# Kernel tuning notes

Measured on AMD Instinct MI355X. Metric: run time of the kernel, lower is better.

Reference implementation:

```python
import jax, jax.numpy as jnp
import numpy as np

GAMMA = 2.0
EPS = 1e-06
LAMBDA_DISTANCE = 1.0
LAMBDA_NORMAL = 0.01
LAMBDA_LAPLACIAN = 0.1
CLS = 1


def vertex_normals(v, f, eps=EPS):
    # v: [N,3], f: [F,3] int. Scatter face normals to vertices, then normalize.
    fv = v[f]  # [F,3,3]
    fn = jnp.cross(fv[:, 1] - fv[:, 0], fv[:, 2] - fv[:, 0])  # [F,3]
    vn = jnp.zeros_like(v)
    vn = vn.at[f[:, 0]].add(fn).at[f[:, 1]].add(fn).at[f[:, 2]].add(fn)
    norm = jnp.maximum(jnp.linalg.norm(vn, axis=-1, keepdims=True), eps)
    return vn / norm


def squared_cdist(a, b):
    # [Na,3] x [Nb,3] -> squared euclidean distances [Na,Nb] (clamped >= 0)
    a2 = jnp.sum(a * a, axis=1)[:, None]
    b2 = jnp.sum(b * b, axis=1)[None, :]
    d2 = a2 + b2 - 2.0 * (a @ b.T)
    return jnp.maximum(d2, 0.0)


def sample_binary_targets(label, v, cls=CLS):
    # Nearest-neighbor grid_sample, align_corners=True, padding zeros.
    # grid = 2*v - 1 -> voxel index = round(v * (size-1)); v[:,0]->W, v[:,1]->H, v[:,2]->D.
    D, H, W = label.shape[2], label.shape[3], label.shape[4]
    ix = jnp.round(v[:, 0] * (W - 1)).astype(jnp.int32)
    iy = jnp.round(v[:, 1] * (H - 1)).astype(jnp.int32)
    iz = jnp.round(v[:, 2] * (D - 1)).astype(jnp.int32)
    inb = (ix >= 0) & (ix < W) & (iy >= 0) & (iy < H) & (iz >= 0) & (iz < D)
    ixc = jnp.clip(ix, 0, W - 1)
    iyc = jnp.clip(iy, 0, H - 1)
    izc = jnp.clip(iz, 0, D - 1)
    vals = (label[0, 0, izc, iyc, ixc] == cls).astype(jnp.float32)
    return jnp.where(inb, vals, 0.0)


def spatial_consistency_loss(rel_pos, targets, gamma=GAMMA, eps=EPS):
    p = jnp.clip(rel_pos, eps, 1.0 - eps)
    pos = targets > 0.5
    pc = jnp.sum(pos).astype(p.dtype)
    tot = jnp.asarray(p.shape[0], p.dtype)
    nc = tot - pc
    alpha = nc / (tot + eps)
    lpos = -alpha * jnp.power(1.0 - p, gamma) * jnp.log(p)
    lneg = -(1.0 - alpha) * jnp.power(p, gamma) * jnp.log(1.0 - p)
    return jnp.sum(jnp.where(pos, lpos, lneg)) / (tot + eps)


def laplacian_uniform(v, f):
    # Uniform mesh Laplacian smoothing: || mean(neighbors) - v ||, averaged.
    i = jnp.concatenate([f[:, 0], f[:, 1], f[:, 2], f[:, 1], f[:, 2], f[:, 0]])
    j = jnp.concatenate([f[:, 1], f[:, 2], f[:, 0], f[:, 0], f[:, 1], f[:, 2]])
    nsum = jnp.zeros_like(v).at[i].add(v[j])
    deg = jnp.zeros((v.shape[0],), v.dtype).at[i].add(1.0)
    lap = nsum / jnp.maximum(deg, 1.0)[:, None] - v
    return jnp.mean(jnp.linalg.norm(lap, axis=1))


def loss_forward(pred_vertices, relative_positions, gt_vertices, pred_faces, gt_faces, label):
    gt_v = jax.lax.stop_gradient(gt_vertices)  # gt comes from label volume; detached in original
    gt_normals = vertex_normals(gt_v, gt_faces)
    # spatial (focal-style) loss
    targets = sample_binary_targets(label, pred_vertices)
    spatial = spatial_consistency_loss(relative_positions, targets)
    # chamfer-style squared surface distance
    d2 = squared_cdist(pred_vertices, gt_v)  # [Np,Ng]
    distance = jnp.mean(jnp.min(d2, axis=1)) + jnp.mean(jnp.min(d2, axis=0))
    # normal consistency vs nearest gt vertex
    pred_normals = vertex_normals(pred_vertices, pred_faces)
    nearest = jnp.argmin(d2, axis=1)
    normal = jnp.mean((pred_normals - gt_normals[nearest]) ** 2)
    # uniform laplacian smoothing
    laplacian = laplacian_uniform(pred_vertices, pred_faces)
    total = spatial + LAMBDA_DISTANCE * distance + LAMBDA_NORMAL * normal + LAMBDA_LAPLACIAN * laplacian
    return total


def setup_inputs() -> dict:
    key = jax.random.key(0)
    k1, k2, k3, k4, k5, k6 = jax.random.split(key, 6)
    Np, Ng = 8192, 12000
    pred_vertices = jax.random.uniform(k1, (Np, 3), dtype=jnp.float32)
    relative_positions = jax.random.uniform(k2, (Np,), dtype=jnp.float32)
    gt_vertices = jax.random.uniform(k3, (Ng, 3), dtype=jnp.float32)
    pred_faces = jax.random.randint(k4, (2 * Np, 3), 0, Np, dtype=jnp.int32)
    gt_faces = jax.random.randint(k5, (2 * Ng, 3), 0, Ng, dtype=jnp.int32)
    label = jax.random.randint(k6, (1, 1, 96, 96, 96), 0, 2, dtype=jnp.int32)
    return {"pred_vertices": pred_vertices, "relative_positions": relative_positions,
            "gt_vertices": gt_vertices, "pred_faces": pred_faces,
            "gt_faces": gt_faces, "label": label}


def reference(pred_vertices, relative_positions, gt_vertices, pred_faces, gt_faces, label):
    return loss_forward(pred_vertices, relative_positions, gt_vertices, pred_faces, gt_faces, label)
```

## Files before the change

### kernel.cpp

```cpp
#include <hip/hip_runtime.h>
#include <math.h>

#define NP 8192
#define NG 12000
#define NFP 16384
#define NFG 24000
#define EPSF 1e-6f

#define GR 16
#define NC (GR*GR*GR)
#define HCELL 0.0625f
#define QL 16
#define QPB (256 / QL)
#define PRED_QBLOCKS (NP / QPB)
#define GT_QBLOCKS (NG / QPB)
#define FACE_BLOCKS ((NFG + NFP + 255) / 256)
#define QF_BLOCKS (PRED_QBLOCKS + GT_QBLOCKS + FACE_BLOCKS)
#define FIN_BLOCKS (NP / 256)

static constexpr size_t OFF_STARTP = 0;
static constexpr size_t OFF_STARTG = 16640;
static constexpr size_t OFF_SORTP  = 33280;
static constexpr size_t OFF_SORTG  = 164352;
static constexpr size_t OFF_GTN    = 356352;
static constexpr size_t OFF_PNN    = 500352;
static constexpr size_t OFF_NSUM   = 598656;
static constexpr size_t OFF_DEG    = 696960;
static constexpr size_t OFF_NEAR   = 729728;
static constexpr size_t OFF_ACCUM  = 762496;
static constexpr size_t OFF_DONE   = 762528;
#define N_ZERO 101545

__device__ __forceinline__ int cell_of(float x) {
    int c = (int)(x * (float)GR);
    return min(max(c, 0), GR - 1);
}

__device__ __forceinline__ void build_cells(const float* __restrict__ pts, int n,
                                            unsigned* __restrict__ start,
                                            float4* __restrict__ sorted,
                                            unsigned* h, unsigned* wsum) {
    int t = threadIdx.x;
    int lane = t & 63, wid = t >> 6;
    for (int i = t; i < NC; i += 1024) h[i] = 0u;
    __syncthreads();
    for (int i = t; i < n; i += 1024) {
        int c = (cell_of(pts[3*i+2]) * GR + cell_of(pts[3*i+1])) * GR + cell_of(pts[3*i]);
        atomicAdd(&h[c], 1u);
    }
    __syncthreads();
    unsigned a0 = h[4*t], a1 = h[4*t+1], a2 = h[4*t+2], a3 = h[4*t+3];
    unsigned tsum = a0 + a1 + a2 + a3;
    unsigned x = tsum;
    #pragma unroll
    for (int off = 1; off < 64; off <<= 1) {
        unsigned y = __shfl_up(x, off, 64);
        if (lane >= off) x += y;
    }
    if (lane == 63) wsum[wid] = x;
    __syncthreads();
    if (t < 16) {
        unsigned w = wsum[t];
        #pragma unroll
        for (int off = 1; off < 16; off <<= 1) {
            unsigned y = __shfl_up(w, off, 64);
            if (t >= off) w += y;
        }
        wsum[t] = w;
    }
    __syncthreads();
    unsigned base = (wid ? wsum[wid-1] : 0u) + (x - tsum);
    unsigned e0 = base, e1 = base + a0, e2 = base + a0 + a1, e3 = base + a0 + a1 + a2;
    start[4*t] = e0; start[4*t+1] = e1; start[4*t+2] = e2; start[4*t+3] = e3;
    h[4*t] = e0; h[4*t+1] = e1; h[4*t+2] = e2; h[4*t+3] = e3;
    __syncthreads();
    for (int i = t; i < n; i += 1024) {
        float px = pts[3*i], py = pts[3*i+1], pz = pts[3*i+2];
        int c = (cell_of(pz) * GR + cell_of(py)) * GR + cell_of(px);
        unsigned pos = atomicAdd(&h[c], 1u);
        sorted[pos] = make_float4(px, py, pz, __int_as_float(i));
    }
    if (t == 0) start[NC] = (unsigned)n;
}

__global__ __launch_bounds__(1024) void build_kernel(const float* __restrict__ pred,
                                                     const float* __restrict__ gt,
                                                     unsigned* __restrict__ startP,
                                                     unsigned* __restrict__ startG,
                                                     float4* __restrict__ sortP,
                                                     float4* __restrict__ sortG,
                                                     float* __restrict__ zero) {
    __shared__ unsigned h[NC];
    __shared__ unsigned wsum[16];
    if (blockIdx.x == 0) {
        build_cells(pred, NP, startP, sortP, h, wsum);
    } else if (blockIdx.x == 1) {
        build_cells(gt, NG, startG, sortG, h, wsum);
    } else {
        int i = (blockIdx.x - 2) * 1024 + threadIdx.x;
        if (i < N_ZERO) zero[i] = 0.0f;
    }
}

__device__ __forceinline__ float wave_sum(float x) {
    #pragma unroll
    for (int o = 32; o > 0; o >>= 1) x += __shfl_down(x, o, 64);
    return x;
}

__device__ __forceinline__ unsigned long long u64min(unsigned long long a,
                                                     unsigned long long b) {
    return a < b ? a : b;
}

__device__ __forceinline__ unsigned long long group_nn(int lane,
                                                       float px, float py, float pz,
                                                       const float4* __restrict__ S,
                                                       const unsigned* __restrict__ cstart) {
    int cx = cell_of(px), cy = cell_of(py), cz = cell_of(pz);
    unsigned long long best = 0xFFFFFFFFFFFFFFFFULL;
    for (int r = 1; ; ++r) {
        int w = 2 * r + 1;
        int nrows = w * w;
        int x0 = max(cx - r, 0), x1 = min(cx + r, GR - 1);
        unsigned long long lb = 0xFFFFFFFFFFFFFFFFULL;
        for (int k = lane; k < nrows; k += QL) {
            int z = cz + k / w - r, y = cy + k % w - r;
            if (z >= 0 && z < GR && y >= 0 && y < GR) {
                int rowbase = (z * GR + y) * GR;
                unsigned s0 = cstart[rowbase + x0];
                unsigned s1 = cstart[rowbase + x1 + 1];
                for (unsigned t = s0; t < s1; ++t) {
                    float4 q = S[t];
                    float ddx = px - q.x, ddy = py - q.y, ddz = pz - q.z;
                    float d2 = fmaf(ddx, ddx, fmaf(ddy, ddy, ddz*ddz));
                    unsigned long long key =
                        ((unsigned long long)__float_as_uint(d2) << 32) |
                        (unsigned)__float_as_int(q.w);
                    lb = u64min(lb, key);
                }
            }
        }
        best = u64min(best, lb);
        #pragma unroll
        for (int m = 1; m < QL; m <<= 1)
            best = u64min(best, (unsigned long long)__shfl_xor((long long)best, m, 64));
        bool covered = (cx - r <= 0) & (cx + r >= GR - 1) &
                       (cy - r <= 0) & (cy + r >= GR - 1) &
                       (cz - r <= 0) & (cz + r >= GR - 1);
        if (covered) break;
        float blo = 1.0e30f;
        if (cx - r > 0)      blo = fminf(blo, px - (float)(cx - r) * HCELL);
        if (cx + r < GR - 1) blo = fminf(blo, (float)(cx + r + 1) * HCELL - px);
        if (cy - r > 0)      blo = fminf(blo, py - (float)(cy - r) * HCELL);
        if (cy + r < GR - 1) blo = fminf(blo, (float)(cy + r + 1) * HCELL - py);
        if (cz - r > 0)      blo = fminf(blo, pz - (float)(cz - r) * HCELL);
        if (cz + r < GR - 1) blo = fminf(blo, (float)(cz + r + 1) * HCELL - pz);
        float bd2 = __uint_as_float((unsigned)(best >> 32));
        if (bd2 <= blo * blo) break;
    }
    return best;
}

__global__ __launch_bounds__(256) void query_face_kernel(const float* __restrict__ pred,
                                                         const int* __restrict__ pf,
                                                         const float* __restrict__ gt,
                                                         const int* __restrict__ gf,
                                                         const float4* __restrict__ sortP,
                                                         const float4* __restrict__ sortG,
                                                         const unsigned* __restrict__ startP,
                                                         const unsigned* __restrict__ startG,
                                                         float* __restrict__ gtn,
                                                         float* __restrict__ pnn,
                                                         float* __restrict__ nsum,
                                                         float* __restrict__ deg,
                                                         int* __restrict__ nearestIdx,
                                                         float* __restrict__ accum) {
    int b = blockIdx.x;
    if (b < PRED_QBLOCKS + GT_QBLOCKS) {
        __shared__ float bs;
        if (threadIdx.x == 0) bs = 0.0f;
        __syncthreads();
        int lane = threadIdx.x & (QL - 1);
        int group = threadIdx.x >> 4;
        float r0 = 0.0f;
        if (b < PRED_QBLOCKS) {
            int qid = b * QPB + group;
            float4 P = sortP[qid];
            unsigned long long key = group_nn(lane, P.x, P.y, P.z, sortG, startG);
            if (lane == 0) {
                int v = __float_as_int(P.w);
                nearestIdx[v] = (int)(unsigned)(key & 0xffffffffu);
                r0 = __uint_as_float((unsigned)(key >> 32));
            }
        } else {
            int qid = (b - PRED_QBLOCKS) * QPB + group;
            float4 Q = sortG[qid];
            unsigned long long key = group_nn(lane, Q.x, Q.y, Q.z, sortP, startP);
            if (lane == 0) r0 = __uint_as_float((unsigned)(key >> 32));
        }
        r0 = wave_sum(r0);
        if ((threadIdx.x & 63) == 0) atomicAdd(&bs, r0);
        __syncthreads();
        if (threadIdx.x == 0)
            atomicAdd(&accum[(b < PRED_QBLOCKS) ? 0 : 6], bs);
    } else {
        int t = (b - PRED_QBLOCKS - GT_QBLOCKS) * 256 + threadIdx.x;
        if (t < NFG) {
            int i0 = gf[3*t], i1 = gf[3*t+1], i2 = gf[3*t+2];
            float ax = gt[3*i0], ay = gt[3*i0+1], az = gt[3*i0+2];
            float bx = gt[3*i1], by = gt[3*i1+1], bz = gt[3*i1+2];
            float cx = gt[3*i2], cy = gt[3*i2+1], cz = gt[3*i2+2];
            float ux = bx-ax, uy = by-ay, uz = bz-az;
            float wx = cx-ax, wy = cy-ay, wz = cz-az;
            float nx = uy*wz - uz*wy, ny = uz*wx - ux*wz, nz = ux*wy - uy*wx;
            atomicAdd(&gtn[3*i0+0], nx); atomicAdd(&gtn[3*i0+1], ny); atomicAdd(&gtn[3*i0+2], nz);
            atomicAdd(&gtn[3*i1+0], nx); atomicAdd(&gtn[3*i1+1], ny); atomicAdd(&gtn[3*i1+2], nz);
            atomicAdd(&gtn[3*i2+0], nx); atomicAdd(&gtn[3*i2+1], ny); atomicAdd(&gtn[3*i2+2], nz);
        } else if (t < NFG + NFP) {
            int u = t - NFG;
            int i0 = pf[3*u], i1 = pf[3*u+1], i2 = pf[3*u+2];
            float ax = pred[3*i0], ay = pred[3*i0+1], az = pred[3*i0+2];
            float bx = pred[3*i1], by = pred[3*i1+1], bz = pred[3*i1+2];
            float cx = pred[3*i2], cy = pred[3*i2+1], cz = pred[3*i2+2];
            float ux = bx-ax, uy = by-ay, uz = bz-az;
            float wx = cx-ax, wy = cy-ay, wz = cz-az;
            float nx = uy*wz - uz*wy, ny = uz*wx - ux*wz, nz = ux*wy - uy*wx;
            atomicAdd(&pnn[3*i0+0], nx); atomicAdd(&pnn[3*i0+1], ny); atomicAdd(&pnn[3*i0+2], nz);
            atomicAdd(&pnn[3*i1+0], nx); atomicAdd(&pnn[3*i1+1], ny); atomicAdd(&pnn[3*i1+2], nz);
            atomicAdd(&pnn[3*i2+0], nx); atomicAdd(&pnn[3*i2+1], ny); atomicAdd(&pnn[3*i2+2], nz);
            atomicAdd(&nsum[3*i0+0], bx+cx); atomicAdd(&nsum[3*i0+1], by+cy); atomicAdd(&nsum[3*i0+2], bz+cz);
            atomicAdd(&nsum[3*i1+0], cx+ax); atomicAdd(&nsum[3*i1+1], cy+ay); atomicAdd(&nsum[3*i1+2], cz+az);
            atomicAdd(&nsum[3*i2+0], ax+bx); atomicAdd(&nsum[3*i2+1], ay+by); atomicAdd(&nsum[3*i2+2], az+bz);
            atomicAdd(&deg[i0], 2.0f); atomicAdd(&deg[i1], 2.0f); atomicAdd(&deg[i2], 2.0f);
        }
    }
}

__global__ __launch_bounds__(256) void finish_kernel(const float* __restrict__ pred,
                                                     const float* __restrict__ relpos,
                                                     const int* __restrict__ label,
                                                     const float* __restrict__ pnn,
                                                     const float* __restrict__ gtn,
                                                     const float* __restrict__ nsum,
                                                     const float* __restrict__ deg,
                                                     const int* __restrict__ nearestIdx,
                                                     float* __restrict__ accum,
                                                     unsigned* __restrict__ done,
                                                     float* __restrict__ out) {
    int v = blockIdx.x * 256 + threadIdx.x;
    float px = pred[3*v], py = pred[3*v+1], pz = pred[3*v+2];
    int nearest = nearestIdx[v];

    float ax = pnn[3*v], ay = pnn[3*v+1], az = pnn[3*v+2];
    float an = fmaxf(sqrtf(ax*ax + ay*ay + az*az), EPSF);
    float gx = gtn[3*nearest], gy = gtn[3*nearest+1], gz = gtn[3*nearest+2];
    float gn = fmaxf(sqrtf(gx*gx + gy*gy + gz*gz), EPSF);
    float nx = ax/an - gx/gn, ny = ay/an - gy/gn, nz = az/an - gz/gn;
    float sse = nx*nx + ny*ny + nz*nz;

    float d = fmaxf(deg[v], 1.0f);
    float lx = nsum[3*v]/d - px, ly = nsum[3*v+1]/d - py, lz = nsum[3*v+2]/d - pz;
    float lapn = sqrtf(lx*lx + ly*ly + lz*lz);

    int ix = (int)rintf(px * 95.0f), iy = (int)rintf(py * 95.0f), iz = (int)rintf(pz * 95.0f);
    bool inb = (ix >= 0) & (ix < 96) & (iy >= 0) & (iy < 96) & (iz >= 0) & (iz < 96);
    int ixc = min(max(ix, 0), 95), iyc = min(max(iy, 0), 95), izc = min(max(iz, 0), 95);
    bool pos = inb && (label[(izc*96 + iyc)*96 + ixc] == 1);

    float p = fminf(fmaxf(relpos[v], EPSF), 1.0f - EPSF);
    float om = 1.0f - p;
    float pcnt = 0.0f, sx = 0.0f, sy = 0.0f;
    if (pos) { pcnt = 1.0f; sx = om*om*logf(p); }
    else     { sy = p*p*logf(om); }

    float r1 = wave_sum(sse), r2 = wave_sum(lapn), r3 = wave_sum(pcnt);
    float r4 = wave_sum(sx),  r5 = wave_sum(sy);
    __shared__ float bsum[5];
    __shared__ bool isLast;
    if (threadIdx.x < 5) bsum[threadIdx.x] = 0.0f;
    __syncthreads();
    if ((threadIdx.x & 63) == 0) {
        atomicAdd(&bsum[0], r1); atomicAdd(&bsum[1], r2); atomicAdd(&bsum[2], r3);
        atomicAdd(&bsum[3], r4); atomicAdd(&bsum[4], r5);
    }
    __syncthreads();
    if (threadIdx.x == 0) {
        atomicAdd(&accum[1], bsum[0]); atomicAdd(&accum[2], bsum[1]);
        atomicAdd(&accum[3], bsum[2]); atomicAdd(&accum[4], bsum[3]);
        atomicAdd(&accum[5], bsum[4]);
        __threadfence();
        unsigned prev = atomicAdd(done, 1u);
        isLast = (prev == FIN_BLOCKS - 1);
    }
    __syncthreads();
    if (isLast && threadIdx.x == 0) {
        __threadfence();
        float sum_row = __hip_atomic_load(&accum[0], __ATOMIC_RELAXED, __HIP_MEMORY_SCOPE_AGENT);
        float sse_t   = __hip_atomic_load(&accum[1], __ATOMIC_RELAXED, __HIP_MEMORY_SCOPE_AGENT);
        float lap_t   = __hip_atomic_load(&accum[2], __ATOMIC_RELAXED, __HIP_MEMORY_SCOPE_AGENT);
        float pc      = __hip_atomic_load(&accum[3], __ATOMIC_RELAXED, __HIP_MEMORY_SCOPE_AGENT);
        float SX      = __hip_atomic_load(&accum[4], __ATOMIC_RELAXED, __HIP_MEMORY_SCOPE_AGENT);
        float SY      = __hip_atomic_load(&accum[5], __ATOMIC_RELAXED, __HIP_MEMORY_SCOPE_AGENT);
        float sum_col = __hip_atomic_load(&accum[6], __ATOMIC_RELAXED, __HIP_MEMORY_SCOPE_AGENT);
        float tot = (float)NP;
        float alpha = (tot - pc) / (tot + EPSF);
        float spatial = (-alpha * SX - (1.0f - alpha) * SY) / (tot + EPSF);
        float distance = sum_row / (float)NP + sum_col / (float)NG;
        float normal = sse_t / (float)(NP * 3);
        float lapm = lap_t / (float)NP;
        out[0] = spatial + 1.0f * distance + 0.01f * normal + 0.1f * lapm;
    }
}

extern "C" void kernel_launch(void* const* d_in, const int* in_sizes, int n_in,
                              void* d_out, int out_size, void* d_ws, size_t ws_size,
                              hipStream_t stream) {
    const float* pred   = (const float*)d_in[0];
    const float* relpos = (const float*)d_in[1];
    const float* gt     = (const float*)d_in[2];
    const int*   pfaces = (const int*)d_in[3];
    const int*   gfaces = (const int*)d_in[4];
    const int*   label  = (const int*)d_in[5];
    float* out = (float*)d_out;

    char* ws = (char*)d_ws;
    unsigned* startP  = (unsigned*)(ws + OFF_STARTP);
    unsigned* startG  = (unsigned*)(ws + OFF_STARTG);
    float4*   sortP   = (float4*)(ws + OFF_SORTP);
    float4*   sortG   = (float4*)(ws + OFF_SORTG);
    float*    gtn     = (float*)(ws + OFF_GTN);
    float*    pnn     = (float*)(ws + OFF_PNN);
    float*    nsum    = (float*)(ws + OFF_NSUM);
    float*    deg     = (float*)(ws + OFF_DEG);
    int*      nearest = (int*)(ws + OFF_NEAR);
    float*    accum   = (float*)(ws + OFF_ACCUM);
    unsigned* done    = (unsigned*)(ws + OFF_DONE);

    int zero_blocks = (N_ZERO + 1023) / 1024;
    hipLaunchKernelGGL(build_kernel, dim3(2 + zero_blocks), dim3(1024), 0, stream,
                       pred, gt, startP, startG, sortP, sortG, (float*)(ws + OFF_GTN));
    hipLaunchKernelGGL(query_face_kernel, dim3(QF_BLOCKS), dim3(256), 0, stream,
                       pred, pfaces, gt, gfaces, sortP, sortG, startP, startG,
                       gtn, pnn, nsum, deg, nearest, accum);
    hipLaunchKernelGGL(finish_kernel, dim3(FIN_BLOCKS), dim3(256), 0, stream,
                       pred, relpos, label, pnn, gtn, nsum, deg, nearest,
                       accum, done, out);
}
```

Baseline: 124.7 us.

## Use one thread per nearest-neighbor query and move pred queries into finish kernel

Replaces the 16-lane cooperative grid search with one thread per query that scans the clamped cell box on its own, dropping the shuffle reductions. The pred→gt nearest-neighbor search moves into the final kernel, which consumes the nearest index directly, so the nearestIdx buffer and its global round trip are gone. The gt queries are no longer read in cell-sorted order but straight from the raw gt array. Per-thread scans can cause load imbalance and divergence inside a wave, and there are fewer blocks in flight during the middle stage.

```diff
diff --git a/kernel.cpp b/kernel.cpp
--- a/kernel.cpp
+++ b/kernel.cpp
@@ -10,13 +10,14 @@
 #define GR 16
 #define NC (GR*GR*GR)
 #define HCELL 0.0625f
-#define QL 16
-#define QPB (256 / QL)
-#define PRED_QBLOCKS (NP / QPB)
-#define GT_QBLOCKS (NG / QPB)
+
+#define N_ZERO 93353
+#define ZERO_BLOCKS ((N_ZERO + 1023) / 1024)
+#define D1_BLOCKS (2 + ZERO_BLOCKS)
+#define GQ_BLOCKS ((NG + 255) / 256)
 #define FACE_BLOCKS ((NFG + NFP + 255) / 256)
-#define QF_BLOCKS (PRED_QBLOCKS + GT_QBLOCKS + FACE_BLOCKS)
-#define FIN_BLOCKS (NP / 256)
+#define MID_BLOCKS (GQ_BLOCKS + FACE_BLOCKS)
+#define PQ_BLOCKS (NP / 256)
 
 static constexpr size_t OFF_STARTP = 0;
 static constexpr size_t OFF_STARTG = 16640;
@@ -26,10 +27,8 @@
 static constexpr size_t OFF_PNN    = 500352;
 static constexpr size_t OFF_NSUM   = 598656;
 static constexpr size_t OFF_DEG    = 696960;
-static constexpr size_t OFF_NEAR   = 729728;
-static constexpr size_t OFF_ACCUM  = 762496;
-static constexpr size_t OFF_DONE   = 762528;
-#define N_ZERO 101545
+static constexpr size_t OFF_ACCUM  = 729728;
+static constexpr size_t OFF_DONE   = 729760;
 
 __device__ __forceinline__ int cell_of(float x) {
     int c = (int)(x * (float)GR);
@@ -113,41 +112,34 @@
     return a < b ? a : b;
 }
 
-__device__ __forceinline__ unsigned long long group_nn(int lane,
-                                                       float px, float py, float pz,
-                                                       const float4* __restrict__ S,
-                                                       const unsigned* __restrict__ cstart) {
+__device__ __forceinline__ unsigned long long pack_key(float px, float py, float pz,
+                                                       float4 q) {
+    float ddx = px - q.x, ddy = py - q.y, ddz = pz - q.z;
+    float d2 = fmaf(ddx, ddx, fmaf(ddy, ddy, ddz*ddz));
+    return ((unsigned long long)__float_as_uint(d2) << 32) |
+           (unsigned)__float_as_int(q.w);
+}
+
+__device__ __forceinline__ unsigned long long lane_nn(float px, float py, float pz,
+                                                      const float4* __restrict__ S,
+                                                      const unsigned* __restrict__ cstart) {
     int cx = cell_of(px), cy = cell_of(py), cz = cell_of(pz);
     unsigned long long best = 0xFFFFFFFFFFFFFFFFULL;
     for (int r = 1; ; ++r) {
-        int w = 2 * r + 1;
-        int nrows = w * w;
         int x0 = max(cx - r, 0), x1 = min(cx + r, GR - 1);
-        unsigned long long lb = 0xFFFFFFFFFFFFFFFFULL;
-        for (int k = lane; k < nrows; k += QL) {
-            int z = cz + k / w - r, y = cy + k % w - r;
-            if (z >= 0 && z < GR && y >= 0 && y < GR) {
+        int y0 = max(cy - r, 0), y1 = min(cy + r, GR - 1);
+        int z0 = max(cz - r, 0), z1 = min(cz + r, GR - 1);
+        for (int z = z0; z <= z1; ++z) {
+            for (int y = y0; y <= y1; ++y) {
                 int rowbase = (z * GR + y) * GR;
                 unsigned s0 = cstart[rowbase + x0];
                 unsigned s1 = cstart[rowbase + x1 + 1];
-                for (unsigned t = s0; t < s1; ++t) {
-                    float4 q = S[t];
-                    float ddx = px - q.x, ddy = py - q.y, ddz = pz - q.z;
-                    float d2 = fmaf(ddx, ddx, fmaf(ddy, ddy, ddz*ddz));
-                    unsigned long long key =
-                        ((unsigned long long)__float_as_uint(d2) << 32) |
-                        (unsigned)__float_as_int(q.w);
-                    lb = u64min(lb, key);
-                }
+                for (unsigned u = s0; u < s1; ++u)
+                    best = u64min(best, pack_key(px, py, pz, S[u]));
             }
         }
-        best = u64min(best, lb);
-        #pragma unroll
-        for (int m = 1; m < QL; m <<= 1)
-            best = u64min(best, (unsigned long long)__shfl_xor((long long)best, m, 64));
-        bool covered = (cx - r <= 0) & (cx + r >= GR - 1) &
-                       (cy - r <= 0) & (cy + r >= GR - 1) &
-                       (cz - r <= 0) & (cz + r >= GR - 1);
+        bool covered = (x0 == 0) & (x1 == GR-1) & (y0 == 0) &
+                       (y1 == GR-1) & (z0 == 0) & (z1 == GR-1);
         if (covered) break;
         float blo = 1.0e30f;
         if (cx - r > 0)      blo = fminf(blo, px - (float)(cx - r) * HCELL);
@@ -162,50 +154,40 @@
     return best;
 }
 
-__global__ __launch_bounds__(256) void query_face_kernel(const float* __restrict__ pred,
-                                                         const int* __restrict__ pf,
-                                                         const float* __restrict__ gt,
-                                                         const int* __restrict__ gf,
-                                                         const float4* __restrict__ sortP,
-                                                         const float4* __restrict__ sortG,
-                                                         const unsigned* __restrict__ startP,
-                                                         const unsigned* __restrict__ startG,
-                                                         float* __restrict__ gtn,
-                                                         float* __restrict__ pnn,
-                                                         float* __restrict__ nsum,
-                                                         float* __restrict__ deg,
-                                                         int* __restrict__ nearestIdx,
-                                                         float* __restrict__ accum) {
+__global__ __launch_bounds__(256) void mid_kernel(const float* __restrict__ pred,
+                                                  const int* __restrict__ pf,
+                                                  const float* __restrict__ gt,
+                                                  const int* __restrict__ gf,
+                                                  const float4* __restrict__ sortP,
+                                                  const unsigned* __restrict__ startP,
+                                                  float* __restrict__ gtn,
+                                                  float* __restrict__ pnn,
+                                                  float* __restrict__ nsum,
+                                                  float* __restrict__ deg,
+                                                  float* __restrict__ accum) {
     int b = blockIdx.x;
-    if (b < PRED_QBLOCKS + GT_QBLOCKS) {
+    if (b < GQ_BLOCKS) {
         __shared__ float bs;
         if (threadIdx.x == 0) bs = 0.0f;
         __syncthreads();
-        int lane = threadIdx.x & (QL - 1);
-        int group = threadIdx.x >> 4;
+        int qid = b * 256 + threadIdx.x;
         float r0 = 0.0f;
-        if (b < PRED_QBLOCKS) {
-            int qid = b * QPB + group;
-            float4 P = sortP[qid];
-            unsigned long long key = group_nn(lane, P.x, P.y, P.z, sortG, startG);
-            if (lane == 0) {
-                int v = __float_as_int(P.w);
-                nearestIdx[v] = (int)(unsigned)(key & 0xffffffffu);
-                r0 = __uint_as_float((unsigned)(key >> 32));
-            }
-        } else {
-            int qid = (b - PRED_QBLOCKS) * QPB + group;
-            float4 Q = sortG[qid];
-            unsigned long long key = group_nn(lane, Q.x, Q.y, Q.z, sortP, startP);
-            if (lane == 0) r0 = __uint_as_float((unsigned)(key >> 32));
+        if (qid < NG) {
+            const float4* SG = (const float4*)nullptr;
+            (void)SG;
+            float gx = gt[0]; (void)gx;
+        }
+        if (qid < NG) {
+            float px = gt[3*qid], py = gt[3*qid+1], pz = gt[3*qid+2];
+            unsigned long long key = lane_nn(px, py, pz, sortP, startP);
+            r0 = __uint_as_float((unsigned)(key >> 32));
         }
         r0 = wave_sum(r0);
         if ((threadIdx.x & 63) == 0) atomicAdd(&bs, r0);
         __syncthreads();
-        if (threadIdx.x == 0)
-            atomicAdd(&accum[(b < PRED_QBLOCKS) ? 0 : 6], bs);
+        if (threadIdx.x == 0) atomicAdd(&accum[6], bs);
     } else {
-        int t = (b - PRED_QBLOCKS - GT_QBLOCKS) * 256 + threadIdx.x;
+        int t = (b - GQ_BLOCKS) * 256 + threadIdx.x;
         if (t < NFG) {
             int i0 = gf[3*t], i1 = gf[3*t+1], i2 = gf[3*t+2];
             float ax = gt[3*i0], ay = gt[3*i0+1], az = gt[3*i0+2];
@@ -237,31 +219,42 @@
     }
 }
 
-__global__ __launch_bounds__(256) void finish_kernel(const float* __restrict__ pred,
-                                                     const float* __restrict__ relpos,
-                                                     const int* __restrict__ label,
-                                                     const float* __restrict__ pnn,
-                                                     const float* __restrict__ gtn,
-                                                     const float* __restrict__ nsum,
-                                                     const float* __restrict__ deg,
-                                                     const int* __restrict__ nearestIdx,
-                                                     float* __restrict__ accum,
-                                                     unsigned* __restrict__ done,
-                                                     float* __restrict__ out) {
-    int v = blockIdx.x * 256 + threadIdx.x;
-    float px = pred[3*v], py = pred[3*v+1], pz = pred[3*v+2];
-    int nearest = nearestIdx[v];
+__global__ __launch_bounds__(256) void pred_kernel(const float* __restrict__ relpos,
+                                                   const int* __restrict__ label,
+                                                   const float4* __restrict__ sortP,
+                                                   const float4* __restrict__ sortG,
+                                                   const unsigned* __restrict__ startG,
+                                                   const float* __restrict__ pnn,
+                                                   const float* __restrict__ gtn,
+                                                   const float* __restrict__ nsum,
+                                                   const float* __restrict__ deg,
+                                                   float* __restrict__ accum,
+                                                   unsigned* __restrict__ done,
+                                                   float* __restrict__ out) {
+    __shared__ float bsum[6];
+    __shared__ bool isLast;
+    int b = blockIdx.x, t = threadIdx.x;
+    if (t < 6) bsum[t] = 0.0f;
+    __syncthreads();
+
+    int qid = b * 256 + t;
+    float4 P = sortP[qid];
+    float px = P.x, py = P.y, pz = P.z;
+    unsigned long long key = lane_nn(px, py, pz, sortG, startG);
+    int v = __float_as_int(P.w);
+    int nearest = (int)(unsigned)(key & 0xffffffffu);
+    float r0 = __uint_as_float((unsigned)(key >> 32));
 
     float ax = pnn[3*v], ay = pnn[3*v+1], az = pnn[3*v+2];
     float an = fmaxf(sqrtf(ax*ax + ay*ay + az*az), EPSF);
     float gx = gtn[3*nearest], gy = gtn[3*nearest+1], gz = gtn[3*nearest+2];
     float gn = fmaxf(sqrtf(gx*gx + gy*gy + gz*gz), EPSF);
     float nx = ax/an - gx/gn, ny = ay/an - gy/gn, nz = az/an - gz/gn;
-    float sse = nx*nx + ny*ny + nz*nz;
+    float r1 = nx*nx + ny*ny + nz*nz;
 
     float d = fmaxf(deg[v], 1.0f);
     float lx = nsum[3*v]/d - px, ly = nsum[3*v+1]/d - py, lz = nsum[3*v+2]/d - pz;
-    float lapn = sqrtf(lx*lx + ly*ly + lz*lz);
+    float r2 = sqrtf(lx*lx + ly*ly + lz*lz);
 
     int ix = (int)rintf(px * 95.0f), iy = (int)rintf(py * 95.0f), iz = (int)rintf(pz * 95.0f);
     bool inb = (ix >= 0) & (ix < 96) & (iy >= 0) & (iy < 96) & (iz >= 0) & (iz < 96);
@@ -270,31 +263,27 @@
 
     float p = fminf(fmaxf(relpos[v], EPSF), 1.0f - EPSF);
     float om = 1.0f - p;
-    float pcnt = 0.0f, sx = 0.0f, sy = 0.0f;
-    if (pos) { pcnt = 1.0f; sx = om*om*logf(p); }
-    else     { sy = p*p*logf(om); }
-
-    float r1 = wave_sum(sse), r2 = wave_sum(lapn), r3 = wave_sum(pcnt);
-    float r4 = wave_sum(sx),  r5 = wave_sum(sy);
-    __shared__ float bsum[5];
-    __shared__ bool isLast;
-    if (threadIdx.x < 5) bsum[threadIdx.x] = 0.0f;
-    __syncthreads();
-    if ((threadIdx.x & 63) == 0) {
-        atomicAdd(&bsum[0], r1); atomicAdd(&bsum[1], r2); atomicAdd(&bsum[2], r3);
-        atomicAdd(&bsum[3], r4); atomicAdd(&bsum[4], r5);
-    }
-    __syncthreads();
-    if (threadIdx.x == 0) {
-        atomicAdd(&accum[1], bsum[0]); atomicAdd(&accum[2], bsum[1]);
-        atomicAdd(&accum[3], bsum[2]); atomicAdd(&accum[4], bsum[3]);
-        atomicAdd(&accum[5], bsum[4]);
+    float r3 = 0.f, r4 = 0.f, r5 = 0.f;
+    if (pos) { r3 = 1.0f; r4 = om*om*logf(p); }
+    else     { r5 = p*p*logf(om); }
+
+    r0 = wave_sum(r0); r1 = wave_sum(r1); r2 = wave_sum(r2);
+    r3 = wave_sum(r3); r4 = wave_sum(r4); r5 = wave_sum(r5);
+    if ((t & 63) == 0) {
+        atomicAdd(&bsum[0], r0); atomicAdd(&bsum[1], r1); atomicAdd(&bsum[2], r2);
+        atomicAdd(&bsum[3], r3); atomicAdd(&bsum[4], r4); atomicAdd(&bsum[5], r5);
+    }
+    __syncthreads();
+    if (t == 0) {
+        atomicAdd(&accum[0], bsum[0]); atomicAdd(&accum[1], bsum[1]);
+        atomicAdd(&accum[2], bsum[2]); atomicAdd(&accum[3], bsum[3]);
+        atomicAdd(&accum[4], bsum[4]); atomicAdd(&accum[5], bsum[5]);
         __threadfence();
         unsigned prev = atomicAdd(done, 1u);
-        isLast = (prev == FIN_BLOCKS - 1);
-    }
-    __syncthreads();
-    if (isLast && threadIdx.x == 0) {
+        isLast = (prev == PQ_BLOCKS - 1);
+    }
+    __syncthreads();
+    if (isLast && t == 0) {
         __threadfence();
         float sum_row = __hip_atomic_load(&accum[0], __ATOMIC_RELAXED, __HIP_MEMORY_SCOPE_AGENT);
         float sse_t   = __hip_atomic_load(&accum[1], __ATOMIC_RELAXED, __HIP_MEMORY_SCOPE_AGENT);
@@ -333,17 +322,16 @@
     float*    pnn     = (float*)(ws + OFF_PNN);
     float*    nsum    = (float*)(ws + OFF_NSUM);
     float*    deg     = (float*)(ws + OFF_DEG);
-    int*      nearest = (int*)(ws + OFF_NEAR);
     float*    accum   = (float*)(ws + OFF_ACCUM);
     unsigned* done    = (unsigned*)(ws + OFF_DONE);
 
-    int zero_blocks = (N_ZERO + 1023) / 1024;
-    hipLaunchKernelGGL(build_kernel, dim3(2 + zero_blocks), dim3(1024), 0, stream,
-                       pred, gt, startP, startG, sortP, sortG, (float*)(ws + OFF_GTN));
-    hipLaunchKernelGGL(query_face_kernel, dim3(QF_BLOCKS), dim3(256), 0, stream,
-                       pred, pfaces, gt, gfaces, sortP, sortG, startP, startG,
-                       gtn, pnn, nsum, deg, nearest, accum);
-    hipLaunchKernelGGL(finish_kernel, dim3(FIN_BLOCKS), dim3(256), 0, stream,
-                       pred, relpos, label, pnn, gtn, nsum, deg, nearest,
-                       accum, done, out);
-}
+    hipLaunchKernelGGL(build_kernel, dim3(D1_BLOCKS), dim3(1024), 0, stream,
+                       pred, gt, startP, startG, sortP, sortG,
+                       (float*)(ws + OFF_GTN));
+    hipLaunchKernelGGL(mid_kernel, dim3(MID_BLOCKS), dim3(256), 0, stream,
+                       pred, pfaces, gt, gfaces, sortP, startP,
+                       gtn, pnn, nsum, deg, accum);
+    hipLaunchKernelGGL(pred_kernel, dim3(PQ_BLOCKS), dim3(256), 0, stream,
+                       relpos, label, sortP, sortG, startG,
+                       pnn, gtn, nsum, deg, accum, done, out);
+}
```

Result: slower. 154.5 us (+23.9%).

## Switch grid nearest-neighbor search from 16-lane groups to one query per thread

Applied to the files above, without the earlier changes.

The nearest-neighbor search now runs one query per thread instead of spreading each query's cell rows across a 16-lane group with shuffle reductions. The first shell (3x3 rows) is unrolled and the outer shells are walked only over clamped ranges. The combined kernel now uses 64-thread blocks, and each wave adds its partial sum atomically instead of reducing through shared memory first. This removes the per-shell cross-lane reductions and the idle lanes on short rows. In exchange it adds per-thread serial work and divergence when neighboring queries need different shell counts, and it issues more global atomics on the accumulators.

```diff
diff --git a/kernel.cpp b/kernel.cpp
--- a/kernel.cpp
+++ b/kernel.cpp
@@ -10,12 +10,16 @@
 #define GR 16
 #define NC (GR*GR*GR)
 #define HCELL 0.0625f
-#define QL 16
-#define QPB (256 / QL)
-#define PRED_QBLOCKS (NP / QPB)
-#define GT_QBLOCKS (NG / QPB)
-#define FACE_BLOCKS ((NFG + NFP + 255) / 256)
-#define QF_BLOCKS (PRED_QBLOCKS + GT_QBLOCKS + FACE_BLOCKS)
+
+#define N_ZERO 101545
+#define ZERO_BLOCKS ((N_ZERO + 1023) / 1024)
+#define D1_BLOCKS (2 + ZERO_BLOCKS)
+
+#define PQB64 (NP / 64)
+#define GQB64 ((NG + 63) / 64)
+#define FQB64 ((NFG + NFP + 63) / 64)
+#define D2_BLOCKS (PQB64 + GQB64 + FQB64)
+
 #define FIN_BLOCKS (NP / 256)
 
 static constexpr size_t OFF_STARTP = 0;
@@ -29,7 +33,6 @@
 static constexpr size_t OFF_NEAR   = 729728;
 static constexpr size_t OFF_ACCUM  = 762496;
 static constexpr size_t OFF_DONE   = 762528;
-#define N_ZERO 101545
 
 __device__ __forceinline__ int cell_of(float x) {
     int c = (int)(x * (float)GR);
@@ -113,41 +116,63 @@
     return a < b ? a : b;
 }
 
-__device__ __forceinline__ unsigned long long group_nn(int lane,
-                                                       float px, float py, float pz,
-                                                       const float4* __restrict__ S,
-                                                       const unsigned* __restrict__ cstart) {
+__device__ __forceinline__ unsigned long long pack_key(float px, float py, float pz,
+                                                       float4 q) {
+    float ddx = px - q.x, ddy = py - q.y, ddz = pz - q.z;
+    float d2 = fmaf(ddx, ddx, fmaf(ddy, ddy, ddz*ddz));
+    return ((unsigned long long)__float_as_uint(d2) << 32) |
+           (unsigned)__float_as_int(q.w);
+}
+
+__device__ unsigned long long lane_nn(float px, float py, float pz,
+                                      const float4* __restrict__ S,
+                                      const unsigned* __restrict__ cstart) {
     int cx = cell_of(px), cy = cell_of(py), cz = cell_of(pz);
     unsigned long long best = 0xFFFFFFFFFFFFFFFFULL;
-    for (int r = 1; ; ++r) {
-        int w = 2 * r + 1;
-        int nrows = w * w;
+    {
+        int x0 = max(cx - 1, 0), x1 = min(cx + 1, GR - 1);
+        #pragma unroll
+        for (int dz = -1; dz <= 1; ++dz) {
+            #pragma unroll
+            for (int dy = -1; dy <= 1; ++dy) {
+                int z = cz + dz, y = cy + dy;
+                if (z >= 0 && z < GR && y >= 0 && y < GR) {
+                    int rowbase = (z * GR + y) * GR;
+                    unsigned s0 = cstart[rowbase + x0];
+                    unsigned s1 = cstart[rowbase + x1 + 1];
+                    for (unsigned u = s0; u < s1; ++u)
+                        best = u64min(best, pack_key(px, py, pz, S[u]));
+                }
+            }
+        }
+        bool covered = (cx - 1 <= 0) & (cx + 1 >= GR - 1) &
+                       (cy - 1 <= 0) & (cy + 1 >= GR - 1) &
+                       (cz - 1 <= 0) & (cz + 1 >= GR - 1);
+        float blo = 1.0e30f;
+        if (cx - 1 > 0)      blo = fminf(blo, px - (float)(cx - 1) * HCELL);
+        if (cx + 1 < GR - 1) blo = fminf(blo, (float)(cx + 2) * HCELL - px);
+        if (cy - 1 > 0)      blo = fminf(blo, py - (float)(cy - 1) * HCELL);
+        if (cy + 1 < GR - 1) blo = fminf(blo, (float)(cy + 2) * HCELL - py);
+        if (cz - 1 > 0)      blo = fminf(blo, pz - (float)(cz - 1) * HCELL);
+        if (cz + 1 < GR - 1) blo = fminf(blo, (float)(cz + 2) * HCELL - pz);
+        float bd2 = __uint_as_float((unsigned)(best >> 32));
+        if (covered || (bd2 <= blo * blo)) return best;
+    }
+    for (int r = 2; ; ++r) {
         int x0 = max(cx - r, 0), x1 = min(cx + r, GR - 1);
-        unsigned long long lb = 0xFFFFFFFFFFFFFFFFULL;
-        for (int k = lane; k < nrows; k += QL) {
-            int z = cz + k / w - r, y = cy + k % w - r;
-            if (z >= 0 && z < GR && y >= 0 && y < GR) {
+        int y0 = max(cy - r, 0), y1 = min(cy + r, GR - 1);
+        int z0 = max(cz - r, 0), z1 = min(cz + r, GR - 1);
+        for (int z = z0; z <= z1; ++z) {
+            for (int y = y0; y <= y1; ++y) {
                 int rowbase = (z * GR + y) * GR;
                 unsigned s0 = cstart[rowbase + x0];
                 unsigned s1 = cstart[rowbase + x1 + 1];
-                for (unsigned t = s0; t < s1; ++t) {
-                    float4 q = S[t];
-                    float ddx = px - q.x, ddy = py - q.y, ddz = pz - q.z;
-                    float d2 = fmaf(ddx, ddx, fmaf(ddy, ddy, ddz*ddz));
-                    unsigned long long key =
-                        ((unsigned long long)__float_as_uint(d2) << 32) |
-                        (unsigned)__float_as_int(q.w);
-                    lb = u64min(lb, key);
-                }
+                for (unsigned u = s0; u < s1; ++u)
+                    best = u64min(best, pack_key(px, py, pz, S[u]));
             }
         }
-        best = u64min(best, lb);
-        #pragma unroll
-        for (int m = 1; m < QL; m <<= 1)
-            best = u64min(best, (unsigned long long)__shfl_xor((long long)best, m, 64));
-        bool covered = (cx - r <= 0) & (cx + r >= GR - 1) &
-                       (cy - r <= 0) & (cy + r >= GR - 1) &
-                       (cz - r <= 0) & (cz + r >= GR - 1);
+        bool covered = (x0 == 0) & (x1 == GR-1) & (y0 == 0) &
+                       (y1 == GR-1) & (z0 == 0) & (z1 == GR-1);
         if (covered) break;
         float blo = 1.0e30f;
         if (cx - r > 0)      blo = fminf(blo, px - (float)(cx - r) * HCELL);
@@ -162,52 +187,43 @@
     return best;
 }
 
-__global__ __launch_bounds__(256) void query_face_kernel(const float* __restrict__ pred,
-                                                         const int* __restrict__ pf,
-                                                         const float* __restrict__ gt,
-                                                         const int* __restrict__ gf,
-                                                         const float4* __restrict__ sortP,
-                                                         const float4* __restrict__ sortG,
-                                                         const unsigned* __restrict__ startP,
-                                                         const unsigned* __restrict__ startG,
-                                                         float* __restrict__ gtn,
-                                                         float* __restrict__ pnn,
-                                                         float* __restrict__ nsum,
-                                                         float* __restrict__ deg,
-                                                         int* __restrict__ nearestIdx,
-                                                         float* __restrict__ accum) {
-    int b = blockIdx.x;
-    if (b < PRED_QBLOCKS + GT_QBLOCKS) {
-        __shared__ float bs;
-        if (threadIdx.x == 0) bs = 0.0f;
-        __syncthreads();
-        int lane = threadIdx.x & (QL - 1);
-        int group = threadIdx.x >> 4;
+__global__ __launch_bounds__(64) void work_kernel(const float* __restrict__ pred,
+                                                  const int* __restrict__ pf,
+                                                  const float* __restrict__ gt,
+                                                  const int* __restrict__ gf,
+                                                  const float4* __restrict__ sortP,
+                                                  const float4* __restrict__ sortG,
+                                                  const unsigned* __restrict__ startP,
+                                                  const unsigned* __restrict__ startG,
+                                                  float* __restrict__ gtn,
+                                                  float* __restrict__ pnn,
+                                                  float* __restrict__ nsum,
+                                                  float* __restrict__ deg,
+                                                  int* __restrict__ nearestIdx,
+                                                  float* __restrict__ accum) {
+    int b = blockIdx.x, t = threadIdx.x;
+    if (b < PQB64) {
+        int qid = b * 64 + t;
+        float4 P = sortP[qid];
+        unsigned long long key = lane_nn(P.x, P.y, P.z, sortG, startG);
+        int v = __float_as_int(P.w);
+        nearestIdx[v] = (int)(unsigned)(key & 0xffffffffu);
+        float r0 = wave_sum(__uint_as_float((unsigned)(key >> 32)));
+        if (t == 0) atomicAdd(&accum[0], r0);
+    } else if (b < PQB64 + GQB64) {
+        int qid = (b - PQB64) * 64 + t;
         float r0 = 0.0f;
-        if (b < PRED_QBLOCKS) {
-            int qid = b * QPB + group;
-            float4 P = sortP[qid];
-            unsigned long long key = group_nn(lane, P.x, P.y, P.z, sortG, startG);
-            if (lane == 0) {
-                int v = __float_as_int(P.w);
-                nearestIdx[v] = (int)(unsigned)(key & 0xffffffffu);
-                r0 = __uint_as_float((unsigned)(key >> 32));
-            }
-        } else {
-            int qid = (b - PRED_QBLOCKS) * QPB + group;
+        if (qid < NG) {
             float4 Q = sortG[qid];
-            unsigned long long key = group_nn(lane, Q.x, Q.y, Q.z, sortP, startP);
-            if (lane == 0) r0 = __uint_as_float((unsigned)(key >> 32));
+            unsigned long long key = lane_nn(Q.x, Q.y, Q.z, sortP, startP);
+            r0 = __uint_as_float((unsigned)(key >> 32));
         }
         r0 = wave_sum(r0);
-        if ((threadIdx.x & 63) == 0) atomicAdd(&bs, r0);
-        __syncthreads();
-        if (threadIdx.x == 0)
-            atomicAdd(&accum[(b < PRED_QBLOCKS) ? 0 : 6], bs);
+        if (t == 0) atomicAdd(&accum[6], r0);
     } else {
-        int t = (b - PRED_QBLOCKS - GT_QBLOCKS) * 256 + threadIdx.x;
-        if (t < NFG) {
-            int i0 = gf[3*t], i1 = gf[3*t+1], i2 = gf[3*t+2];
+        int f = (b - PQB64 - GQB64) * 64 + t;
+        if (f < NFG) {
+            int i0 = gf[3*f], i1 = gf[3*f+1], i2 = gf[3*f+2];
             float ax = gt[3*i0], ay = gt[3*i0+1], az = gt[3*i0+2];
             float bx = gt[3*i1], by = gt[3*i1+1], bz = gt[3*i1+2];
             float cx = gt[3*i2], cy = gt[3*i2+1], cz = gt[3*i2+2];
@@ -217,8 +233,8 @@
             atomicAdd(&gtn[3*i0+0], nx); atomicAdd(&gtn[3*i0+1], ny); atomicAdd(&gtn[3*i0+2], nz);
             atomicAdd(&gtn[3*i1+0], nx); atomicAdd(&gtn[3*i1+1], ny); atomicAdd(&gtn[3*i1+2], nz);
             atomicAdd(&gtn[3*i2+0], nx); atomicAdd(&gtn[3*i2+1], ny); atomicAdd(&gtn[3*i2+2], nz);
-        } else if (t < NFG + NFP) {
-            int u = t - NFG;
+        } else if (f < NFG + NFP) {
+            int u = f - NFG;
             int i0 = pf[3*u], i1 = pf[3*u+1], i2 = pf[3*u+2];
             float ax = pred[3*i0], ay = pred[3*i0+1], az = pred[3*i0+2];
             float bx = pred[3*i1], by = pred[3*i1+1], bz = pred[3*i1+2];
@@ -337,10 +353,10 @@
     float*    accum   = (float*)(ws + OFF_ACCUM);
     unsigned* done    = (unsigned*)(ws + OFF_DONE);
 
-    int zero_blocks = (N_ZERO + 1023) / 1024;
-    hipLaunchKernelGGL(build_kernel, dim3(2 + zero_blocks), dim3(1024), 0, stream,
-                       pred, gt, startP, startG, sortP, sortG, (float*)(ws + OFF_GTN));
-    hipLaunchKernelGGL(query_face_kernel, dim3(QF_BLOCKS), dim3(256), 0, stream,
+    hipLaunchKernelGGL(build_kernel, dim3(D1_BLOCKS), dim3(1024), 0, stream,
+                       pred, gt, startP, startG, sortP, sortG,
+                       (float*)(ws + OFF_GTN));
+    hipLaunchKernelGGL(work_kernel, dim3(D2_BLOCKS), dim3(64), 0, stream,
                        pred, pfaces, gt, gfaces, sortP, sortG, startP, startG,
                        gtn, pnn, nsum, deg, nearest, accum);
     hipLaunchKernelGGL(finish_kernel, dim3(FIN_BLOCKS), dim3(256), 0, stream,
```

Result: slower. 144.0 us (+15.5%).
